# Kernel optimization log

Hardware: AMD Instinct MI355X
Metric: run time of the kernel (lower is better)

Reference implementation:

```python
import jax, jax.numpy as jnp
import numpy as np

BATCH, SEQ, DIM = 4, 4096, 2048
NUM_EXPERTS, TOP_K, RANK = 8, 2, 16
SCALING = 1.0


def setup_inputs() -> dict:
    key = jax.random.key(0)
    k0, k1, k2, k3 = jax.random.split(key, 4)
    s = 0.02
    x = jax.random.normal(k0, (BATCH, SEQ, DIM), dtype=jnp.float32)
    gate_W = jax.random.normal(k1, (NUM_EXPERTS, DIM), dtype=jnp.float32) * s  # [E, D] torch Linear layout
    gate_b = jnp.zeros((NUM_EXPERTS,), dtype=jnp.float32)
    A = jax.random.normal(k2, (NUM_EXPERTS, RANK, DIM), dtype=jnp.float32) * s   # lora_A weights [E, R, D]
    Bm = jax.random.normal(k3, (NUM_EXPERTS, DIM, RANK), dtype=jnp.float32) * s  # lora_B weights [E, D, R]
    return {"x": x, "gate_W": gate_W, "gate_b": gate_b, "A": A, "Bm": Bm}


def reference(x, gate_W, gate_b, A, Bm):
    # Gate: logits [B, S, E], softmax probs
    logits = jnp.einsum('bsd,ed->bse', x, gate_W) + gate_b
    gate_probs = jax.nn.softmax(logits, axis=-1)
    # Top-k selection. NOTE: the original torch code computes topk weights but
    # NEVER uses them -- expert outputs are summed unweighted over the top-k set.
    _, idx = jax.lax.top_k(gate_probs, TOP_K)  # idx: [B, S, K]
    # mask[b,s,e] = expert e is in token (b,s)'s top-k
    mask = jnp.any(idx[..., :, None] == jnp.arange(NUM_EXPERTS), axis=-2)  # [B, S, E] bool
    # Dense grouped LoRA: h [B, S, E, R] (small, rank=16), masked before combine
    h = jnp.einsum('bsd,erd->bser', x, A)
    h = jax.nn.gelu(h, approximate=False) * mask[..., None].astype(x.dtype)
    out = jnp.einsum('bser,edr->bsd', h, Bm) * SCALING  # [B, S, D]
    return out, gate_probs
```

## Files before the change

kernel.cpp:

```cpp
#include <hip/hip_runtime.h>
#include <math.h>

#define NTOK 16384
#define DIM  2048
#define NEXP 8
#define RANK 16

typedef unsigned short ushort_t;
typedef unsigned int   uint_t;
typedef __attribute__((ext_vector_type(8))) short bf16x8;
typedef __attribute__((ext_vector_type(4))) float f32x4;

__device__ __forceinline__ ushort_t f2bf(float f) {
  union { float f; uint_t u; } v; v.f = f;
  uint_t r = (v.u + 0x7FFFu + ((v.u >> 16) & 1u)) >> 16;
  return (ushort_t)r;
}
__device__ __forceinline__ float bf2f(ushort_t s) {
  union { uint_t u; float f; } v; v.u = ((uint_t)s) << 16;
  return v.f;
}

__global__ __launch_bounds__(256) void k0_prep(
    const float* __restrict__ gW, const float* __restrict__ A,
    const float* __restrict__ Bm,
    ushort_t* __restrict__ W1, ushort_t* __restrict__ Wgl,
    ushort_t* __restrict__ Bm2) {
  int b = blockIdx.x, t = threadIdx.x;
  if (b < 1152) {
    int idx = b * 256 + t;
    int row = idx >> 11, col = idx & 2047;
    float v = (row < 8) ? gW[row * 2048 + col]
            : (row < 16) ? 0.f
            : A[(size_t)(row - 16) * 2048 + col];
    W1[idx] = f2bf(v);
  } else if (b < 1280) {
    int idx = (b - 1152) * 256 + t;
    int row = idx >> 11, col = idx & 2047;
    float v = (row < 8) ? gW[row * 2048 + col] : 0.f;
    ushort_t hi = f2bf(v);
    Wgl[idx] = f2bf(v - bf2f(hi));
  } else {
    int idx = (b - 1280) * 256 + t;
    int d = idx >> 7, c = idx & 127, e = c >> 4, r = c & 15;
    Bm2[idx] = f2bf(Bm[((size_t)e * 2048 + d) * 16 + r]);
  }
}

#define BK  64
#define BKP 72

__global__ __launch_bounds__(256) void k1_gate_h(
    const float* __restrict__ x, const float* __restrict__ gate_b,
    const ushort_t* __restrict__ W1, const ushort_t* __restrict__ Wgl,
    ushort_t* __restrict__ Hm, float* __restrict__ probs) {
  __shared__ __align__(16) ushort_t xs_hi[32][BKP];
  __shared__ __align__(16) ushort_t xs_lo[32][BKP];
  __shared__ __align__(16) ushort_t wh[144][BKP];
  __shared__ __align__(16) ushort_t wl[16][BKP];
  __shared__ float Cs[32][152];
  __shared__ int sel0s[32], sel1s[32];

  const int t = threadIdx.x;
  const int lane = t & 63, wave = t >> 6;
  const int l15 = lane & 15, q = lane >> 4;
  const int mt = wave & 1;
  const int ng = wave >> 1;
  const int ntiles = ng ? 5 : 4;
  const int tok0 = blockIdx.x * 32;

  f32x4 acc[5];
  #pragma unroll
  for (int i = 0; i < 5; ++i) acc[i] = (f32x4)0.f;

  const float4* xg = (const float4*)(x + (size_t)tok0 * DIM);
  const uint2* wg1 = (const uint2*)W1;
  const uint2* wgl = (const uint2*)Wgl;

  for (int ch = 0; ch < 32; ++ch) {
    const int k0 = ch * BK;
    #pragma unroll
    for (int i = 0; i < 2; ++i) {
      int idx = t + i * 256;
      int row = idx >> 4, c4 = idx & 15;
      float4 v = xg[row * (DIM / 4) + (k0 >> 2) + c4];
      float vv[4] = {v.x, v.y, v.z, v.w};
      ushort_t h4[4], l4[4];
      #pragma unroll
      for (int j = 0; j < 4; ++j) {
        h4[j] = f2bf(vv[j]);
        l4[j] = f2bf(vv[j] - bf2f(h4[j]));
      }
      *(uint2*)&xs_hi[row][c4 * 4] = *(const uint2*)h4;
      *(uint2*)&xs_lo[row][c4 * 4] = *(const uint2*)l4;
    }
    #pragma unroll
    for (int i = 0; i < 9; ++i) {
      int idx = t + i * 256;
      int row = idx >> 4, c = idx & 15;
      uint2 v = wg1[row * (DIM / 4) + (k0 >> 2) + c];
      *(uint2*)&wh[row][c * 4] = v;
    }
    {
      int row = t >> 4, c = t & 15;
      uint2 v = wgl[row * (DIM / 4) + (k0 >> 2) + c];
      *(uint2*)&wl[row][c * 4] = v;
    }
    __syncthreads();

    #pragma unroll
    for (int kk = 0; kk < BK; kk += 32) {
      bf16x8 ah = *(const bf16x8*)&xs_hi[mt * 16 + l15][kk + q * 8];
      if (ng == 0) {
        bf16x8 al  = *(const bf16x8*)&xs_lo[mt * 16 + l15][kk + q * 8];
        bf16x8 bgl = *(const bf16x8*)&wl[l15][kk + q * 8];
        bf16x8 b0  = *(const bf16x8*)&wh[l15][kk + q * 8];
        acc[0] = __builtin_amdgcn_mfma_f32_16x16x32_bf16(ah, b0, acc[0], 0, 0, 0);
        acc[0] = __builtin_amdgcn_mfma_f32_16x16x32_bf16(al, b0, acc[0], 0, 0, 0);
        acc[0] = __builtin_amdgcn_mfma_f32_16x16x32_bf16(ah, bgl, acc[0], 0, 0, 0);
        #pragma unroll
        for (int nt = 1; nt < 4; ++nt) {
          bf16x8 b = *(const bf16x8*)&wh[nt * 16 + l15][kk + q * 8];
          acc[nt] = __builtin_amdgcn_mfma_f32_16x16x32_bf16(ah, b, acc[nt], 0, 0, 0);
        }
      } else {
        #pragma unroll
        for (int nt = 0; nt < 5; ++nt) {
          bf16x8 b = *(const bf16x8*)&wh[64 + nt * 16 + l15][kk + q * 8];
          acc[nt] = __builtin_amdgcn_mfma_f32_16x16x32_bf16(ah, b, acc[nt], 0, 0, 0);
        }
      }
    }
    __syncthreads();
  }

  const int colbase = ng ? 64 : 0;
  #pragma unroll
  for (int i = 0; i < 5; ++i) {
    if (i < ntiles) {
      #pragma unroll
      for (int r = 0; r < 4; ++r)
        Cs[mt * 16 + q * 4 + r][colbase + i * 16 + l15] = acc[i][r];
    }
  }
  __syncthreads();

  if (t < 32) {
    int m = t;
    float lg[NEXP];
    #pragma unroll
    for (int e = 0; e < NEXP; ++e) lg[e] = Cs[m][e] + gate_b[e];
    float mx = lg[0];
    #pragma unroll
    for (int e = 1; e < NEXP; ++e) mx = fmaxf(mx, lg[e]);
    float ex[NEXP], s = 0.f;
    #pragma unroll
    for (int e = 0; e < NEXP; ++e) { ex[e] = __expf(lg[e] - mx); s += ex[e]; }
    float inv = 1.f / s;
    float4 p0 = make_float4(ex[0] * inv, ex[1] * inv, ex[2] * inv, ex[3] * inv);
    float4 p1 = make_float4(ex[4] * inv, ex[5] * inv, ex[6] * inv, ex[7] * inv);
    float* pp = probs + (size_t)(tok0 + m) * NEXP;
    *(float4*)pp = p0; *(float4*)(pp + 4) = p1;
    int i0 = 0;
    #pragma unroll
    for (int e = 1; e < NEXP; ++e) if (lg[e] > lg[i0]) i0 = e;
    int i1 = (i0 == 0) ? 1 : 0;
    #pragma unroll
    for (int e = 0; e < NEXP; ++e) if (e != i0 && lg[e] > lg[i1]) i1 = e;
    sel0s[m] = i0; sel1s[m] = i1;
  }
  __syncthreads();

  {
    int m = t >> 3, e = t & 7;
    int on = (e == sel0s[m]) | (e == sel1s[m]);
    ushort_t ov[16];
    #pragma unroll
    for (int r = 0; r < RANK; ++r) {
      float v = Cs[m][16 + e * 16 + r];
      float g = on ? (0.5f * v * (1.f + erff(v * 0.70710678118654752f))) : 0.f;
      ov[r] = f2bf(g);
    }
    ushort_t* hp = Hm + ((size_t)(tok0 + m) * 128 + e * 16);
    *(uint4*)hp       = *(const uint4*)&ov[0];
    *(uint4*)(hp + 8) = *(const uint4*)&ov[8];
  }
}

__global__ __launch_bounds__(64) void k2_combine(
    const ushort_t* __restrict__ Hm, const ushort_t* __restrict__ Bm2,
    float* __restrict__ out) {
  const int lane = threadIdx.x;
  const int l15 = lane & 15, q = lane >> 4;
  const int t0 = blockIdx.x * 64;
  const int nb = blockIdx.y * 256;

  bf16x8 a[4][4];
  #pragma unroll
  for (int mt = 0; mt < 4; ++mt)
    #pragma unroll
    for (int kk = 0; kk < 4; ++kk)
      a[mt][kk] = *(const bf16x8*)&Hm[(size_t)(t0 + mt * 16 + l15) * 128 + kk * 32 + q * 8];

  for (int i = 0; i < 16; ++i) {
    int n0 = nb + i * 16;
    bf16x8 b0 = *(const bf16x8*)&Bm2[(size_t)(n0 + l15) * 128 + 0 * 32 + q * 8];
    bf16x8 b1 = *(const bf16x8*)&Bm2[(size_t)(n0 + l15) * 128 + 1 * 32 + q * 8];
    bf16x8 b2 = *(const bf16x8*)&Bm2[(size_t)(n0 + l15) * 128 + 2 * 32 + q * 8];
    bf16x8 b3 = *(const bf16x8*)&Bm2[(size_t)(n0 + l15) * 128 + 3 * 32 + q * 8];
    #pragma unroll
    for (int mt = 0; mt < 4; ++mt) {
      f32x4 c = (f32x4)0.f;
      c = __builtin_amdgcn_mfma_f32_16x16x32_bf16(a[mt][0], b0, c, 0, 0, 0);
      c = __builtin_amdgcn_mfma_f32_16x16x32_bf16(a[mt][1], b1, c, 0, 0, 0);
      c = __builtin_amdgcn_mfma_f32_16x16x32_bf16(a[mt][2], b2, c, 0, 0, 0);
      c = __builtin_amdgcn_mfma_f32_16x16x32_bf16(a[mt][3], b3, c, 0, 0, 0);
      #pragma unroll
      for (int r = 0; r < 4; ++r)
        out[(size_t)(t0 + mt * 16 + q * 4 + r) * DIM + n0 + l15] = c[r];
    }
  }
}

extern "C" void kernel_launch(void* const* d_in, const int* in_sizes, int n_in,
                              void* d_out, int out_size, void* d_ws, size_t ws_size,
                              hipStream_t stream) {
  const float* x      = (const float*)d_in[0];
  const float* gate_W = (const float*)d_in[1];
  const float* gate_b = (const float*)d_in[2];
  const float* A      = (const float*)d_in[3];
  const float* Bm     = (const float*)d_in[4];

  float* out   = (float*)d_out;
  float* probs = out + (size_t)NTOK * DIM;

  ushort_t* W1  = (ushort_t*)d_ws;
  ushort_t* Wgl = W1 + 144 * 2048;
  ushort_t* Bm2 = Wgl + 16 * 2048;
  ushort_t* Hm  = Bm2 + 2048 * 128;

  k0_prep<<<dim3(2304), dim3(256), 0, stream>>>(gate_W, A, Bm, W1, Wgl, Bm2);
  k1_gate_h<<<dim3(NTOK / 32), dim3(256), 0, stream>>>(x, gate_b, W1, Wgl, Hm, probs);
  k2_combine<<<dim3(NTOK / 64, DIM / 256), dim3(64), 0, stream>>>(Hm, Bm2, out);
}
```

Baseline: 308.6 us.

## Double-buffer gate/LoRA-A GEMM with direct global-to-LDS weight loads and swizzled layout

Repacks the gate, LoRA-A and gate-residual weights into per-chunk, XOR-swizzled tiles, so k1 can stage them straight into LDS with global_load_lds. k1 becomes double-buffered: the next chunk's x and weights are prefetched while MFMAs run on the current buffer, and one barrier per chunk replaces two. k2 halves its token tile to get more blocks and software-pipelines its B fragment loads. The cost is roughly doubled LDS use in k1, which may reduce occupancy, and more index arithmetic for the swizzle.

```diff
diff --git a/kernel.cpp b/kernel.cpp
--- a/kernel.cpp
+++ b/kernel.cpp
@@ -21,43 +21,45 @@
   return v.f;
 }
 
+__device__ __forceinline__ void gl_lds16(const ushort_t* g, ushort_t* l) {
+  __builtin_amdgcn_global_load_lds(
+      (const __attribute__((address_space(1))) unsigned int*)g,
+      (__attribute__((address_space(3))) unsigned int*)l, 16, 0, 0);
+}
+
 __global__ __launch_bounds__(256) void k0_prep(
     const float* __restrict__ gW, const float* __restrict__ A,
     const float* __restrict__ Bm,
-    ushort_t* __restrict__ W1, ushort_t* __restrict__ Wgl,
-    ushort_t* __restrict__ Bm2) {
+    ushort_t* __restrict__ Wc, ushort_t* __restrict__ Bm2) {
   int b = blockIdx.x, t = threadIdx.x;
-  if (b < 1152) {
+  if (b < 1280) {
     int idx = b * 256 + t;
-    int row = idx >> 11, col = idx & 2047;
-    float v = (row < 8) ? gW[row * 2048 + col]
-            : (row < 16) ? 0.f
-            : A[(size_t)(row - 16) * 2048 + col];
-    W1[idx] = f2bf(v);
-  } else if (b < 1280) {
-    int idx = (b - 1152) * 256 + t;
-    int row = idx >> 11, col = idx & 2047;
-    float v = (row < 8) ? gW[row * 2048 + col] : 0.f;
-    ushort_t hi = f2bf(v);
-    Wgl[idx] = f2bf(v - bf2f(hi));
+    int r = idx >> 11, d = idx & 2047;
+    float v;
+    if (r < 8)        v = gW[r * 2048 + d];
+    else if (r < 16)  v = 0.f;
+    else if (r < 144) v = A[(size_t)(r - 16) * 2048 + d];
+    else if (r < 152) { float g = gW[(r - 144) * 2048 + d]; v = g - bf2f(f2bf(g)); }
+    else              v = 0.f;
+    int ch = d >> 6, c = d & 63;
+    int cs = ((((c >> 3) ^ (r & 7)) << 3) | (c & 7));
+    Wc[((size_t)ch * 160 + r) * 64 + cs] = f2bf(v);
   } else {
     int idx = (b - 1280) * 256 + t;
-    int d = idx >> 7, c = idx & 127, e = c >> 4, r = c & 15;
-    Bm2[idx] = f2bf(Bm[((size_t)e * 2048 + d) * 16 + r]);
-  }
-}
-
-#define BK  64
+    int dd = idx >> 7, c = idx & 127, e = c >> 4, rr = c & 15;
+    Bm2[idx] = f2bf(Bm[((size_t)e * 2048 + dd) * 16 + rr]);
+  }
+}
+
 #define BKP 72
 
 __global__ __launch_bounds__(256) void k1_gate_h(
     const float* __restrict__ x, const float* __restrict__ gate_b,
-    const ushort_t* __restrict__ W1, const ushort_t* __restrict__ Wgl,
+    const ushort_t* __restrict__ Wc,
     ushort_t* __restrict__ Hm, float* __restrict__ probs) {
-  __shared__ __align__(16) ushort_t xs_hi[32][BKP];
-  __shared__ __align__(16) ushort_t xs_lo[32][BKP];
-  __shared__ __align__(16) ushort_t wh[144][BKP];
-  __shared__ __align__(16) ushort_t wl[16][BKP];
+  __shared__ __align__(16) ushort_t ws_w[2][160 * 64];
+  __shared__ __align__(16) ushort_t xs_hi[2][32][BKP];
+  __shared__ __align__(16) ushort_t xs_lo[2][32][BKP];
   __shared__ float Cs[32][152];
   __shared__ int sel0s[32], sel1s[32];
 
@@ -74,63 +76,78 @@
   for (int i = 0; i < 5; ++i) acc[i] = (f32x4)0.f;
 
   const float4* xg = (const float4*)(x + (size_t)tok0 * DIM);
-  const uint2* wg1 = (const uint2*)W1;
-  const uint2* wgl = (const uint2*)Wgl;
-
-  for (int ch = 0; ch < 32; ++ch) {
-    const int k0 = ch * BK;
+  const int xrow0 = t >> 4, xc4 = t & 15;
+
+  float4 xv[2];
+
+  auto load_x = [&](int ch) {
+    xv[0] = xg[xrow0 * (DIM / 4) + ch * 16 + xc4];
+    xv[1] = xg[(16 + xrow0) * (DIM / 4) + ch * 16 + xc4];
+  };
+  auto stage_w = [&](int ch, int buf) {
+    const ushort_t* src = Wc + (size_t)ch * (160 * 64);
+    #pragma unroll
+    for (int i = 0; i < 5; ++i)
+      gl_lds16(src + (size_t)(i * 256 + t) * 8,
+               &ws_w[buf][(i * 256 + wave * 64) * 8]);
+  };
+  auto write_x = [&](int buf) {
     #pragma unroll
     for (int i = 0; i < 2; ++i) {
-      int idx = t + i * 256;
-      int row = idx >> 4, c4 = idx & 15;
-      float4 v = xg[row * (DIM / 4) + (k0 >> 2) + c4];
-      float vv[4] = {v.x, v.y, v.z, v.w};
+      int row = xrow0 + i * 16;
+      float vv[4] = {xv[i].x, xv[i].y, xv[i].z, xv[i].w};
       ushort_t h4[4], l4[4];
       #pragma unroll
       for (int j = 0; j < 4; ++j) {
         h4[j] = f2bf(vv[j]);
         l4[j] = f2bf(vv[j] - bf2f(h4[j]));
       }
-      *(uint2*)&xs_hi[row][c4 * 4] = *(const uint2*)h4;
-      *(uint2*)&xs_lo[row][c4 * 4] = *(const uint2*)l4;
-    }
-    #pragma unroll
-    for (int i = 0; i < 9; ++i) {
-      int idx = t + i * 256;
-      int row = idx >> 4, c = idx & 15;
-      uint2 v = wg1[row * (DIM / 4) + (k0 >> 2) + c];
-      *(uint2*)&wh[row][c * 4] = v;
-    }
-    {
-      int row = t >> 4, c = t & 15;
-      uint2 v = wgl[row * (DIM / 4) + (k0 >> 2) + c];
-      *(uint2*)&wl[row][c * 4] = v;
-    }
-    __syncthreads();
-
-    #pragma unroll
-    for (int kk = 0; kk < BK; kk += 32) {
-      bf16x8 ah = *(const bf16x8*)&xs_hi[mt * 16 + l15][kk + q * 8];
+      *(uint2*)&xs_hi[buf][row][xc4 * 4] = *(const uint2*)h4;
+      *(uint2*)&xs_lo[buf][row][xc4 * 4] = *(const uint2*)l4;
+    }
+  };
+
+  load_x(0);
+  stage_w(0, 0);
+  write_x(0);
+  __syncthreads();
+
+  for (int ch = 0; ch < 32; ++ch) {
+    const int cur = ch & 1, nxt = cur ^ 1;
+    if (ch < 31) { load_x(ch + 1); stage_w(ch + 1, nxt); }
+
+    const ushort_t* wb = ws_w[cur];
+    auto wfrag = [&](int r, int kkg) -> bf16x8 {
+      int pos = (r << 3) + ((kkg + q) ^ (r & 7));
+      return *(const bf16x8*)&wb[pos << 3];
+    };
+
+    #pragma unroll
+    for (int kk = 0; kk < 64; kk += 32) {
+      const int kkg = kk >> 3;
+      bf16x8 ah = *(const bf16x8*)&xs_hi[cur][mt * 16 + l15][kk + q * 8];
       if (ng == 0) {
-        bf16x8 al  = *(const bf16x8*)&xs_lo[mt * 16 + l15][kk + q * 8];
-        bf16x8 bgl = *(const bf16x8*)&wl[l15][kk + q * 8];
-        bf16x8 b0  = *(const bf16x8*)&wh[l15][kk + q * 8];
+        bf16x8 al  = *(const bf16x8*)&xs_lo[cur][mt * 16 + l15][kk + q * 8];
+        bf16x8 bgl = wfrag(144 + l15, kkg);
+        bf16x8 b0  = wfrag(l15, kkg);
         acc[0] = __builtin_amdgcn_mfma_f32_16x16x32_bf16(ah, b0, acc[0], 0, 0, 0);
         acc[0] = __builtin_amdgcn_mfma_f32_16x16x32_bf16(al, b0, acc[0], 0, 0, 0);
         acc[0] = __builtin_amdgcn_mfma_f32_16x16x32_bf16(ah, bgl, acc[0], 0, 0, 0);
         #pragma unroll
         for (int nt = 1; nt < 4; ++nt) {
-          bf16x8 b = *(const bf16x8*)&wh[nt * 16 + l15][kk + q * 8];
+          bf16x8 b = wfrag(nt * 16 + l15, kkg);
           acc[nt] = __builtin_amdgcn_mfma_f32_16x16x32_bf16(ah, b, acc[nt], 0, 0, 0);
         }
       } else {
         #pragma unroll
         for (int nt = 0; nt < 5; ++nt) {
-          bf16x8 b = *(const bf16x8*)&wh[64 + nt * 16 + l15][kk + q * 8];
+          bf16x8 b = wfrag(64 + nt * 16 + l15, kkg);
           acc[nt] = __builtin_amdgcn_mfma_f32_16x16x32_bf16(ah, b, acc[nt], 0, 0, 0);
         }
       }
     }
+
+    if (ch < 31) write_x(nxt);
     __syncthreads();
   }
 
@@ -192,33 +209,44 @@
     float* __restrict__ out) {
   const int lane = threadIdx.x;
   const int l15 = lane & 15, q = lane >> 4;
-  const int t0 = blockIdx.x * 64;
+  const int t0 = blockIdx.x * 32;
   const int nb = blockIdx.y * 256;
 
-  bf16x8 a[4][4];
-  #pragma unroll
-  for (int mt = 0; mt < 4; ++mt)
+  bf16x8 a[2][4];
+  #pragma unroll
+  for (int mt = 0; mt < 2; ++mt)
     #pragma unroll
     for (int kk = 0; kk < 4; ++kk)
       a[mt][kk] = *(const bf16x8*)&Hm[(size_t)(t0 + mt * 16 + l15) * 128 + kk * 32 + q * 8];
 
-  for (int i = 0; i < 16; ++i) {
-    int n0 = nb + i * 16;
-    bf16x8 b0 = *(const bf16x8*)&Bm2[(size_t)(n0 + l15) * 128 + 0 * 32 + q * 8];
-    bf16x8 b1 = *(const bf16x8*)&Bm2[(size_t)(n0 + l15) * 128 + 1 * 32 + q * 8];
-    bf16x8 b2 = *(const bf16x8*)&Bm2[(size_t)(n0 + l15) * 128 + 2 * 32 + q * 8];
-    bf16x8 b3 = *(const bf16x8*)&Bm2[(size_t)(n0 + l15) * 128 + 3 * 32 + q * 8];
-    #pragma unroll
-    for (int mt = 0; mt < 4; ++mt) {
+  const ushort_t* bp = Bm2 + (size_t)(nb + l15) * 128 + q * 8;
+
+  auto loadB = [&](bf16x8* dst, int i) {
+    #pragma unroll
+    for (int k = 0; k < 4; ++k)
+      dst[k] = *(const bf16x8*)(bp + (size_t)i * 2048 + k * 32);
+  };
+  auto comp = [&](const bf16x8* bb, int i) {
+    #pragma unroll
+    for (int mt = 0; mt < 2; ++mt) {
       f32x4 c = (f32x4)0.f;
-      c = __builtin_amdgcn_mfma_f32_16x16x32_bf16(a[mt][0], b0, c, 0, 0, 0);
-      c = __builtin_amdgcn_mfma_f32_16x16x32_bf16(a[mt][1], b1, c, 0, 0, 0);
-      c = __builtin_amdgcn_mfma_f32_16x16x32_bf16(a[mt][2], b2, c, 0, 0, 0);
-      c = __builtin_amdgcn_mfma_f32_16x16x32_bf16(a[mt][3], b3, c, 0, 0, 0);
+      #pragma unroll
+      for (int k = 0; k < 4; ++k)
+        c = __builtin_amdgcn_mfma_f32_16x16x32_bf16(a[mt][k], bb[k], c, 0, 0, 0);
       #pragma unroll
       for (int r = 0; r < 4; ++r)
-        out[(size_t)(t0 + mt * 16 + q * 4 + r) * DIM + n0 + l15] = c[r];
-    }
+        out[(size_t)(t0 + mt * 16 + q * 4 + r) * DIM + nb + i * 16 + l15] = c[r];
+    }
+  };
+
+  bf16x8 bA[4], bB[4];
+  loadB(bA, 0);
+  #pragma unroll
+  for (int ii = 0; ii < 8; ++ii) {
+    loadB(bB, 2 * ii + 1);
+    comp(bA, 2 * ii);
+    if (ii < 7) loadB(bA, 2 * ii + 2);
+    comp(bB, 2 * ii + 1);
   }
 }
 
@@ -234,12 +262,11 @@
   float* out   = (float*)d_out;
   float* probs = out + (size_t)NTOK * DIM;
 
-  ushort_t* W1  = (ushort_t*)d_ws;
-  ushort_t* Wgl = W1 + 144 * 2048;
-  ushort_t* Bm2 = Wgl + 16 * 2048;
+  ushort_t* Wc  = (ushort_t*)d_ws;
+  ushort_t* Bm2 = Wc + 32 * 160 * 64;
   ushort_t* Hm  = Bm2 + 2048 * 128;
 
-  k0_prep<<<dim3(2304), dim3(256), 0, stream>>>(gate_W, A, Bm, W1, Wgl, Bm2);
-  k1_gate_h<<<dim3(NTOK / 32), dim3(256), 0, stream>>>(x, gate_b, W1, Wgl, Hm, probs);
-  k2_combine<<<dim3(NTOK / 64, DIM / 256), dim3(64), 0, stream>>>(Hm, Bm2, out);
-}
+  k0_prep<<<dim3(2304), dim3(256), 0, stream>>>(gate_W, A, Bm, Wc, Bm2);
+  k1_gate_h<<<dim3(NTOK / 32), dim3(256), 0, stream>>>(x, gate_b, Wc, Hm, probs);
+  k2_combine<<<dim3(NTOK / 32, DIM / 256), dim3(64), 0, stream>>>(Hm, Bm2, out);
+}
```

Result: no change. 314.5 us (+1.9%).
